# Kernel tuning notes

Hardware: AMD Instinct MI355X
Metric: run time of the kernel (lower is better)

## Reference

```python
import jax, jax.numpy as jnp
import numpy as np

ROUTING_ITERS = 3
EPS = 1e-12


def squash(s):
    # squash over both pose-matrix dims (axis=[-2,-1])
    n2 = jnp.sum(s * s, axis=(-2, -1), keepdims=True)
    n = jnp.sqrt(n2 + EPS)
    return s * (n2 / (1.0 + n2)) / n


def setup_inputs() -> dict:
    key = jax.random.key(0)
    k1, k2, k3 = jax.random.split(key, 3)
    B, I, O = 32, 4096, 32
    input_poses = jax.random.normal(k1, (B, I, 4, 4), dtype=jnp.float32)
    input_activations = jax.random.uniform(k2, (B, I), dtype=jnp.float32)
    # weight: [num_capsules, num_input_caps, 4, 4] (trans_in=trans_out=False for 4x4->4x4)
    w = jax.random.normal(k3, (O, I, 4, 4), dtype=jnp.float32) * 0.05
    return {"input_poses": input_poses, "input_activations": input_activations, "w": w}


def reference(input_poses, input_activations, w):
    # votes: expand_dims(poses,1) @ w, broadcast over output capsules -> [B,O,I,4,4]
    votes = jnp.einsum("bixy,oiyz->boixz", input_poses, w)
    B, O, I = votes.shape[0], votes.shape[1], votes.shape[2]

    # dynamic routing (routing-by-agreement)
    b = jnp.zeros((B, O, I), dtype=votes.dtype)
    s = None
    for it in range(ROUTING_ITERS):
        c = jax.nn.softmax(b, axis=1)  # couple over output capsules
        s = jnp.einsum("boi,boixy->boxy", c, votes)  # weighted sum [B,O,4,4]
        if it < ROUTING_ITERS - 1:
            v = squash(s)
            b = b + jnp.einsum("boixy,boxy->boi", votes, v)

    capsule_poses = squash(s)  # activation == 'squash'
    capsule_activations = jnp.sqrt(jnp.sum(capsule_poses * capsule_poses, axis=(-2, -1)) + EPS)
    return capsule_poses, capsule_activations
```

## Files before the change

### kernel.cpp

```cpp
#include <hip/hip_runtime.h>
#include <hip/hip_cooperative_groups.h>
#include <math.h>


#define NB 32
#define NI 4096
#define NO 32
#define I_TILE 16
#define NCHUNK (NI / I_TILE)
#define B_TILE 8
#define NBG (NB / B_TILE)
#define SOFF (NB * NO * 16)
#define EPSF 1e-12f

#define W_OSTR 10
#define W_ISTR (32 * W_OSTR)
#define W_WORDS (I_TILE * W_ISTR)
#define P_WORDS (B_TILE * I_TILE * 8)

namespace cg = cooperative_groups;

typedef _Float16 v2h __attribute__((ext_vector_type(2)));

#if __has_builtin(__builtin_amdgcn_fdot2)
__device__ __forceinline__ float fdot2(v2h a, v2h b, float c) {
    return __builtin_amdgcn_fdot2(a, b, c, false);
}
#else
__device__ __forceinline__ float fdot2(v2h a, v2h b, float c) {
    return fmaf((float)a.x, (float)b.x, fmaf((float)a.y, (float)b.y, c));
}
#endif

#if __has_builtin(__builtin_amdgcn_cvt_pkrtz)
__device__ __forceinline__ v2h pk2h(float a, float b) {
    return __builtin_bit_cast(v2h, __builtin_amdgcn_cvt_pkrtz(a, b));
}
#else
__device__ __forceinline__ v2h pk2h(float a, float b) {
    v2h r; r.x = (_Float16)a; r.y = (_Float16)b; return r;
}
#endif

__device__ __forceinline__ v2h bch(unsigned u) {
    return __builtin_bit_cast(v2h, u);
}

__device__ __forceinline__ float dot4(const float4 a, const float4 b) {
    return fmaf(a.x, b.x, fmaf(a.y, b.y, fmaf(a.z, b.z, a.w * b.w)));
}

__device__ __forceinline__ void fma4(float4& s, const float c, const float4 t) {
    s.x = fmaf(c, t.x, s.x);
    s.y = fmaf(c, t.y, s.y);
    s.z = fmaf(c, t.z, s.z);
    s.w = fmaf(c, t.w, s.w);
}

__device__ __forceinline__ void add4(float4& s, const float4 t) {
    s.x += t.x; s.y += t.y; s.z += t.z; s.w += t.w;
}

template <int CTRL>
__device__ __forceinline__ float dpp_add(float x) {
    int xi = __builtin_bit_cast(int, x);
    int yi = __builtin_amdgcn_update_dpp(0, xi, CTRL, 0xf, 0xf, false);
    return x + __builtin_bit_cast(float, yi);
}

__device__ __forceinline__ float sum32(float x) {
    x = dpp_add<0xB1>(x);
    x = dpp_add<0x4E>(x);
    x = dpp_add<0x141>(x);
    x = dpp_add<0x140>(x);
#if __has_builtin(__builtin_amdgcn_permlane16_swap)
    typedef unsigned uv2 __attribute__((ext_vector_type(2)));
    const unsigned xi = __builtin_bit_cast(unsigned, x);
    uv2 r = __builtin_amdgcn_permlane16_swap(xi, xi, false, false);
    return __builtin_bit_cast(float, r.x) + __builtin_bit_cast(float, r.y);
#else
    int t = __builtin_amdgcn_ds_swizzle(__builtin_bit_cast(int, x), 0x401F);
    return x + __builtin_bit_cast(float, t);
#endif
}

__global__ __launch_bounds__(256, 4) void caps_fused(
    const float* __restrict__ poses, const float* __restrict__ w,
    float* __restrict__ s_part, float* __restrict__ v_contrib,
    float* __restrict__ out)
{
    __shared__ unsigned wsw[W_WORDS];
    __shared__ unsigned psw[P_WORDS];
    __shared__ float red[16][17];

    const int tid    = threadIdx.x;
    const int chunk  = blockIdx.x;
    const int bgroup = blockIdx.y;
    const int ibase  = chunk * I_TILE;

    #pragma unroll
    for (int r = 0; r < 4; ++r) {
        const int idx = r * 256 + tid;
        const int o_l = idx >> 5;
        const int l   = idx & 31;
        const int i_l = l >> 1;
        const int m   = l & 1;
        const float* g = w + (((size_t)o_l * NI + ibase + i_l) << 4) + (m << 3);
        const float4 A = *(const float4*)g;
        const float4 B = *(const float4*)(g + 4);
        const v2h c0 = pk2h(A.x, B.x), c1 = pk2h(A.y, B.y);
        const v2h c2 = pk2h(A.z, B.z), c3 = pk2h(A.w, B.w);
        const int base = i_l * W_ISTR + o_l * W_OSTR + (m << 2);
        *(uint2*)&wsw[base]     = make_uint2(__builtin_bit_cast(unsigned, c0),
                                             __builtin_bit_cast(unsigned, c1));
        *(uint2*)&wsw[base + 2] = make_uint2(__builtin_bit_cast(unsigned, c2),
                                             __builtin_bit_cast(unsigned, c3));
    }
    #pragma unroll
    for (int r = 0; r < 2; ++r) {
        const int idx = r * 256 + tid;
        const int b_l = idx >> 6;
        const int l   = idx & 63;
        const int i_l = l >> 2;
        const int x   = l & 3;
        const float4 row = *(const float4*)(
            poses + (((size_t)(bgroup * B_TILE + b_l) * NI + ibase + i_l) << 4)
                  + (x << 2));
        const v2h c0 = pk2h(row.x, row.y), c1 = pk2h(row.z, row.w);
        *(uint2*)&psw[((b_l * I_TILE + i_l) << 3) + (x << 1)] =
            make_uint2(__builtin_bit_cast(unsigned, c0),
                       __builtin_bit_cast(unsigned, c1));
    }

    const int o    = tid & 31;
    const int bsub = tid >> 5;
    const int b    = bgroup * B_TILE + bsub;
    const int bo   = b * NO + o;
    const int rbo  = bgroup * NCHUNK + chunk;

    const unsigned* wrow = &wsw[o * W_OSTR];
    const unsigned* prow = &psw[(bsub * I_TILE) << 3];

    float4 vv0 = {0,0,0,0}, vv1 = {0,0,0,0}, vv2 = {0,0,0,0}, vv3 = {0,0,0,0};

    cg::grid_group gg = cg::this_grid();

    __syncthreads();

    for (int pass = 0; pass < 3; ++pass) {
        float4 s0 = {0,0,0,0}, s1 = {0,0,0,0}, s2 = {0,0,0,0}, s3 = {0,0,0,0};

        #pragma unroll 2
        for (int i = 0; i < I_TILE; ++i) {
            const uint2 wa = *(const uint2*)&wrow[i * W_ISTR + 0];
            const uint2 wb = *(const uint2*)&wrow[i * W_ISTR + 2];
            const uint2 wc = *(const uint2*)&wrow[i * W_ISTR + 4];
            const uint2 wd = *(const uint2*)&wrow[i * W_ISTR + 6];
            const uint4 pa = *(const uint4*)&prow[(i << 3) + 0];
            const uint4 pb = *(const uint4*)&prow[(i << 3) + 4];

            const v2h p00 = bch(pa.x), p01 = bch(pa.y);
            const v2h p10 = bch(pa.z), p11 = bch(pa.w);
            const v2h p20 = bch(pb.x), p21 = bch(pb.y);
            const v2h p30 = bch(pb.z), p31 = bch(pb.w);
            const v2h w00 = bch(wa.x), w01 = bch(wa.y);
            const v2h w02 = bch(wb.x), w03 = bch(wb.y);
            const v2h w10 = bch(wc.x), w11 = bch(wc.y);
            const v2h w12 = bch(wd.x), w13 = bch(wd.y);

            float4 t0, t1, t2, t3;
            t0.x = fdot2(p00, w00, fdot2(p01, w10, 0.0f));
            t0.y = fdot2(p00, w01, fdot2(p01, w11, 0.0f));
            t0.z = fdot2(p00, w02, fdot2(p01, w12, 0.0f));
            t0.w = fdot2(p00, w03, fdot2(p01, w13, 0.0f));
            t1.x = fdot2(p10, w00, fdot2(p11, w10, 0.0f));
            t1.y = fdot2(p10, w01, fdot2(p11, w11, 0.0f));
            t1.z = fdot2(p10, w02, fdot2(p11, w12, 0.0f));
            t1.w = fdot2(p10, w03, fdot2(p11, w13, 0.0f));
            t2.x = fdot2(p20, w00, fdot2(p21, w10, 0.0f));
            t2.y = fdot2(p20, w01, fdot2(p21, w11, 0.0f));
            t2.z = fdot2(p20, w02, fdot2(p21, w12, 0.0f));
            t2.w = fdot2(p20, w03, fdot2(p21, w13, 0.0f));
            t3.x = fdot2(p30, w00, fdot2(p31, w10, 0.0f));
            t3.y = fdot2(p30, w01, fdot2(p31, w11, 0.0f));
            t3.z = fdot2(p30, w02, fdot2(p31, w12, 0.0f));
            t3.w = fdot2(p30, w03, fdot2(p31, w13, 0.0f));

            float cc;
            if (pass == 0) {
                cc = 1.0f / 32.0f;
            } else {
                const float d = dot4(t0,vv0) + dot4(t1,vv1)
                              + dot4(t2,vv2) + dot4(t3,vv3);
                const float e  = __expf(d);
                const float es = sum32(e);
                cc = __fdividef(e, es);
            }
            fma4(s0, cc, t0); fma4(s1, cc, t1);
            fma4(s2, cc, t2); fma4(s3, cc, t3);
        }

        float4* sp = (float4*)(s_part + (((size_t)bo * NCHUNK + chunk) << 4));
        sp[0] = s0; sp[1] = s1; sp[2] = s2; sp[3] = s3;

        __threadfence();
        gg.sync();
        __threadfence();

        {
            const int k   = tid & 15;
            const int grp = tid >> 4;
            const float* base = s_part + ((size_t)rbo << 12);
            float acc = 0.0f;
            #pragma unroll
            for (int j = 0; j < 16; ++j)
                acc += base[((grp + (j << 4)) << 4) + k];
            red[grp][k] = acc;
        }
        __syncthreads();
        if (tid < 16) {
            float a = red[0][tid];
            #pragma unroll
            for (int g2 = 1; g2 < 16; ++g2) a += red[g2][tid];
            float x = a * a;
            #pragma unroll
            for (int msk = 8; msk >= 1; msk >>= 1)
                x += __shfl_xor(x, msk, 16);
            const float n2 = x;
            const float n  = sqrtf(n2 + EPSF);
            const float sc = (n2 / (1.0f + n2)) / n;
            if (pass < 2) {
                v_contrib[(rbo << 4) + tid] = sc * a;
            } else {
                out[(rbo << 4) + tid] = sc * a;
                if (tid == 0)
                    out[NB * NO * 16 + rbo] = sqrtf(n2 * sc * sc + EPSF);
            }
        }
        if (pass == 2) break;

        __threadfence();
        gg.sync();
        __threadfence();

        const float4* vp = (const float4*)(v_contrib + (bo << 4));
        add4(vv0, vp[0]); add4(vv1, vp[1]);
        add4(vv2, vp[2]); add4(vv3, vp[3]);
    }
}

__global__ __launch_bounds__(256, 4) void caps_pass_h(
    const float* __restrict__ poses, const float* __restrict__ w,
    const float* __restrict__ v_buf, float* __restrict__ s_part,
    const int pass)
{
    __shared__ unsigned wsw[W_WORDS];
    __shared__ unsigned psw[P_WORDS];
    const int tid    = threadIdx.x;
    const int chunk  = blockIdx.x;
    const int bgroup = blockIdx.y;
    const int ibase  = chunk * I_TILE;

    #pragma unroll
    for (int r = 0; r < 4; ++r) {
        const int idx = r * 256 + tid;
        const int o_l = idx >> 5;
        const int l   = idx & 31;
        const int i_l = l >> 1;
        const int m   = l & 1;
        const float* g = w + (((size_t)o_l * NI + ibase + i_l) << 4) + (m << 3);
        const float4 A = *(const float4*)g;
        const float4 B = *(const float4*)(g + 4);
        const v2h c0 = pk2h(A.x, B.x), c1 = pk2h(A.y, B.y);
        const v2h c2 = pk2h(A.z, B.z), c3 = pk2h(A.w, B.w);
        const int base = i_l * W_ISTR + o_l * W_OSTR + (m << 2);
        *(uint2*)&wsw[base]     = make_uint2(__builtin_bit_cast(unsigned, c0),
                                             __builtin_bit_cast(unsigned, c1));
        *(uint2*)&wsw[base + 2] = make_uint2(__builtin_bit_cast(unsigned, c2),
                                             __builtin_bit_cast(unsigned, c3));
    }
    #pragma unroll
    for (int r = 0; r < 2; ++r) {
        const int idx = r * 256 + tid;
        const int b_l = idx >> 6;
        const int l   = idx & 63;
        const int i_l = l >> 2;
        const int x   = l & 3;
        const float4 row = *(const float4*)(
            poses + (((size_t)(bgroup * B_TILE + b_l) * NI + ibase + i_l) << 4)
                  + (x << 2));
        const v2h c0 = pk2h(row.x, row.y), c1 = pk2h(row.z, row.w);
        *(uint2*)&psw[((b_l * I_TILE + i_l) << 3) + (x << 1)] =
            make_uint2(__builtin_bit_cast(unsigned, c0),
                       __builtin_bit_cast(unsigned, c1));
    }

    const int o    = tid & 31;
    const int bsub = tid >> 5;
    const int b    = bgroup * B_TILE + bsub;
    const int bo   = b * NO + o;

    float4 vv0 = {0,0,0,0}, vv1 = {0,0,0,0}, vv2 = {0,0,0,0}, vv3 = {0,0,0,0};
    if (pass > 0) {
        const float4* vp = (const float4*)(v_buf + (bo << 4));
        vv0 = vp[0]; vv1 = vp[1]; vv2 = vp[2]; vv3 = vp[3];
    }

    const unsigned* wrow = &wsw[o * W_OSTR];
    const unsigned* prow = &psw[(bsub * I_TILE) << 3];

    __syncthreads();

    float4 s0 = {0,0,0,0}, s1 = {0,0,0,0}, s2 = {0,0,0,0}, s3 = {0,0,0,0};

    #pragma unroll 2
    for (int i = 0; i < I_TILE; ++i) {
        const uint2 wa = *(const uint2*)&wrow[i * W_ISTR + 0];
        const uint2 wb = *(const uint2*)&wrow[i * W_ISTR + 2];
        const uint2 wc = *(const uint2*)&wrow[i * W_ISTR + 4];
        const uint2 wd = *(const uint2*)&wrow[i * W_ISTR + 6];
        const uint4 pa = *(const uint4*)&prow[(i << 3) + 0];
        const uint4 pb = *(const uint4*)&prow[(i << 3) + 4];

        const v2h p00 = bch(pa.x), p01 = bch(pa.y);
        const v2h p10 = bch(pa.z), p11 = bch(pa.w);
        const v2h p20 = bch(pb.x), p21 = bch(pb.y);
        const v2h p30 = bch(pb.z), p31 = bch(pb.w);
        const v2h w00 = bch(wa.x), w01 = bch(wa.y);
        const v2h w02 = bch(wb.x), w03 = bch(wb.y);
        const v2h w10 = bch(wc.x), w11 = bch(wc.y);
        const v2h w12 = bch(wd.x), w13 = bch(wd.y);

        float4 t0, t1, t2, t3;
        t0.x = fdot2(p00, w00, fdot2(p01, w10, 0.0f));
        t0.y = fdot2(p00, w01, fdot2(p01, w11, 0.0f));
        t0.z = fdot2(p00, w02, fdot2(p01, w12, 0.0f));
        t0.w = fdot2(p00, w03, fdot2(p01, w13, 0.0f));
        t1.x = fdot2(p10, w00, fdot2(p11, w10, 0.0f));
        t1.y = fdot2(p10, w01, fdot2(p11, w11, 0.0f));
        t1.z = fdot2(p10, w02, fdot2(p11, w12, 0.0f));
        t1.w = fdot2(p10, w03, fdot2(p11, w13, 0.0f));
        t2.x = fdot2(p20, w00, fdot2(p21, w10, 0.0f));
        t2.y = fdot2(p20, w01, fdot2(p21, w11, 0.0f));
        t2.z = fdot2(p20, w02, fdot2(p21, w12, 0.0f));
        t2.w = fdot2(p20, w03, fdot2(p21, w13, 0.0f));
        t3.x = fdot2(p30, w00, fdot2(p31, w10, 0.0f));
        t3.y = fdot2(p30, w01, fdot2(p31, w11, 0.0f));
        t3.z = fdot2(p30, w02, fdot2(p31, w12, 0.0f));
        t3.w = fdot2(p30, w03, fdot2(p31, w13, 0.0f));

        float cc;
        if (pass == 0) {
            cc = 1.0f / 32.0f;
        } else {
            const float d = dot4(t0,vv0) + dot4(t1,vv1)
                          + dot4(t2,vv2) + dot4(t3,vv3);
            const float e  = __expf(d);
            const float es = sum32(e);
            cc = __fdividef(e, es);
        }
        fma4(s0, cc, t0); fma4(s1, cc, t1);
        fma4(s2, cc, t2); fma4(s3, cc, t3);
    }

    float4* sp = (float4*)(s_part + ((size_t)chunk * (NB * NO) + bo) * 16);
    sp[0] = s0; sp[1] = s1; sp[2] = s2; sp[3] = s3;
}

__global__ __launch_bounds__(256) void caps_reduce(
    const float* __restrict__ s_part, float* __restrict__ v_buf,
    float* __restrict__ out, const int pass)
{
    const int e  = threadIdx.x & 63;
    const int c4 = threadIdx.x >> 6;
    const int eg = blockIdx.x * 64 + e;

    float acc = 0.0f;
    #pragma unroll 8
    for (int j = 0; j < NCHUNK / 4; ++j) {
        const int c = c4 * (NCHUNK / 4) + j;
        acc += s_part[(size_t)c * SOFF + eg];
    }
    __shared__ float red[4][64];
    red[c4][e] = acc;
    __syncthreads();

    if (threadIdx.x < 64) {
        const float a = red[0][e] + red[1][e] + red[2][e] + red[3][e];
        float x = a * a;
        #pragma unroll
        for (int msk = 8; msk >= 1; msk >>= 1)
            x += __shfl_xor(x, msk, 16);
        const float n2 = x;
        const float n  = sqrtf(n2 + EPSF);
        const float sc = (n2 / (1.0f + n2)) / n;
        if (pass < 2) {
            const float vold = (pass == 0) ? 0.0f : v_buf[eg];
            v_buf[eg] = fmaf(sc, a, vold);
        } else {
            out[eg] = sc * a;
            if ((e & 15) == 0)
                out[NB * NO * 16 + (eg >> 4)] = sqrtf(n2 * sc * sc + EPSF);
        }
    }
}

#define FB_CHUNKS 32
#define FB_IPB (NI / FB_CHUNKS)

__device__ __forceinline__ float4 row_mm(const float4 p, const float4 w0,
                                         const float4 w1, const float4 w2,
                                         const float4 w3) {
    float4 r;
    r.x = fmaf(p.x, w0.x, fmaf(p.y, w1.x, fmaf(p.z, w2.x, p.w * w3.x)));
    r.y = fmaf(p.x, w0.y, fmaf(p.y, w1.y, fmaf(p.z, w2.y, p.w * w3.y)));
    r.z = fmaf(p.x, w0.z, fmaf(p.y, w1.z, fmaf(p.z, w2.z, p.w * w3.z)));
    r.w = fmaf(p.x, w0.w, fmaf(p.y, w1.w, fmaf(p.z, w2.w, p.w * w3.w)));
    return r;
}

__global__ __launch_bounds__(256) void caps_pass_fb(
    const float* __restrict__ poses, const float* __restrict__ w,
    const float* __restrict__ v_buf, float* __restrict__ s_buf, const int mode)
{
    const int tid   = threadIdx.x;
    const int b     = blockIdx.y;
    const int chunk = blockIdx.x;
    const int o     = tid & 31;
    const int g     = tid >> 5;

    float4 v0 = {0,0,0,0}, v1 = {0,0,0,0}, v2 = {0,0,0,0}, v3 = {0,0,0,0};
    if (mode != 0) {
        const float4* vp = (const float4*)(v_buf + (((b * NO) + o) << 4));
        v0 = vp[0]; v1 = vp[1]; v2 = vp[2]; v3 = vp[3];
    }
    float4 s0 = {0,0,0,0}, s1 = {0,0,0,0}, s2 = {0,0,0,0}, s3 = {0,0,0,0};
    const int ibase = chunk * FB_IPB + g;
    #pragma unroll 4
    for (int it = 0; it < FB_IPB / 8; ++it) {
        const int i = ibase + (it << 3);
        const float4* ppf = (const float4*)(poses + ((((size_t)b * NI) + i) << 4));
        const float4 p0 = ppf[0], p1 = ppf[1], p2 = ppf[2], p3 = ppf[3];
        const float4* wpf = (const float4*)(w + ((((size_t)o * NI) + i) << 4));
        const float4 w0 = wpf[0], w1 = wpf[1], w2 = wpf[2], w3 = wpf[3];
        const float4 t0 = row_mm(p0, w0, w1, w2, w3);
        const float4 t1 = row_mm(p1, w0, w1, w2, w3);
        const float4 t2 = row_mm(p2, w0, w1, w2, w3);
        const float4 t3 = row_mm(p3, w0, w1, w2, w3);
        float cc;
        if (mode == 0) {
            cc = 1.0f / 32.0f;
        } else {
            float d = dot4(t0,v0) + dot4(t1,v1) + dot4(t2,v2) + dot4(t3,v3);
            const float e  = __expf(d);
            const float es = sum32(e);
            cc = __fdividef(e, es);
        }
        fma4(s0, cc, t0); fma4(s1, cc, t1);
        fma4(s2, cc, t2); fma4(s3, cc, t3);
    }
    __shared__ float red[8][32][16];
    float4* rp = (float4*)&red[g][o][0];
    rp[0] = s0; rp[1] = s1; rp[2] = s2; rp[3] = s3;
    __syncthreads();
    for (int idx = tid; idx < NO * 16; idx += 256) {
        const int oo = idx >> 4;
        const int k  = idx & 15;
        float acc = red[0][oo][k];
        #pragma unroll
        for (int gg = 1; gg < 8; ++gg) acc += red[gg][oo][k];
        atomicAdd(&s_buf[(((b * NO) + oo) << 4) + k], acc);
    }
}

__global__ __launch_bounds__(256) void caps_squash_fb(
    float* __restrict__ s_buf, float* __restrict__ v_buf,
    float* __restrict__ out, const int mode)
{
    const int idx = blockIdx.x * 256 + threadIdx.x;
    if (idx >= NB * NO) return;
    float4* sp = (float4*)(s_buf + (idx << 4));
    const float4 s0 = sp[0], s1 = sp[1], s2 = sp[2], s3 = sp[3];
    const float n2 = dot4(s0,s0) + dot4(s1,s1) + dot4(s2,s2) + dot4(s3,s3);
    const float n  = sqrtf(n2 + EPSF);
    const float sc = (n2 / (1.0f + n2)) / n;
    if (mode == 2) {
        float4* op = (float4*)(out + (idx << 4));
        op[0] = make_float4(sc*s0.x, sc*s0.y, sc*s0.z, sc*s0.w);
        op[1] = make_float4(sc*s1.x, sc*s1.y, sc*s1.z, sc*s1.w);
        op[2] = make_float4(sc*s2.x, sc*s2.y, sc*s2.z, sc*s2.w);
        op[3] = make_float4(sc*s3.x, sc*s3.y, sc*s3.z, sc*s3.w);
        out[NB * NO * 16 + idx] = sqrtf(n2 * sc * sc + EPSF);
    } else {
        float4* vp = (float4*)(v_buf + (idx << 4));
        float4 a0 = {0,0,0,0}, a1 = {0,0,0,0}, a2 = {0,0,0,0}, a3 = {0,0,0,0};
        if (mode != 0) { a0 = vp[0]; a1 = vp[1]; a2 = vp[2]; a3 = vp[3]; }
        vp[0] = make_float4(fmaf(sc,s0.x,a0.x), fmaf(sc,s0.y,a0.y), fmaf(sc,s0.z,a0.z), fmaf(sc,s0.w,a0.w));
        vp[1] = make_float4(fmaf(sc,s1.x,a1.x), fmaf(sc,s1.y,a1.y), fmaf(sc,s1.z,a1.z), fmaf(sc,s1.w,a1.w));
        vp[2] = make_float4(fmaf(sc,s2.x,a2.x), fmaf(sc,s2.y,a2.y), fmaf(sc,s2.z,a2.z), fmaf(sc,s2.w,a2.w));
        vp[3] = make_float4(fmaf(sc,s3.x,a3.x), fmaf(sc,s3.y,a3.y), fmaf(sc,s3.z,a3.z), fmaf(sc,s3.w,a3.w));
        const float4 z = {0,0,0,0};
        sp[0] = z; sp[1] = z; sp[2] = z; sp[3] = z;
    }
}

extern "C" void kernel_launch(void* const* d_in, const int* in_sizes, int n_in,
                              void* d_out, int out_size, void* d_ws, size_t ws_size,
                              hipStream_t stream) {
    (void)in_sizes; (void)n_in; (void)out_size;
    const float* poses = (const float*)d_in[0];
    const float* w     = (const float*)d_in[2];
    float* out = (float*)d_out;

    const size_t need = ((size_t)NCHUNK * SOFF + SOFF) * sizeof(float);
    if (ws_size >= need) {
        float* s_part = (float*)d_ws;
        float* v_buf  = s_part + (size_t)NCHUNK * SOFF;

        static int coop_state = -1;
        if (coop_state != 0) {
            void* args[] = { (void*)&poses, (void*)&w, (void*)&s_part,
                             (void*)&v_buf, (void*)&out };
            hipError_t e = hipLaunchCooperativeKernel(
                caps_fused, dim3(NCHUNK, NBG), dim3(256), args, 0u, stream);
            if (e == hipSuccess) { coop_state = 1; return; }
            coop_state = 0;
            (void)hipGetLastError();
        }

        dim3 gp(NCHUNK, NBG), blk(256), gr(256);
        for (int pass = 0; pass < 3; ++pass) {
            caps_pass_h<<<gp, blk, 0, stream>>>(poses, w, v_buf, s_part, pass);
            caps_reduce<<<gr, blk, 0, stream>>>(s_part, v_buf, out, pass);
        }
    } else {
        float* s_buf = (float*)d_ws;
        float* v_buf = s_buf + SOFF;
        (void)hipMemsetAsync(s_buf, 0, SOFF * sizeof(float), stream);
        dim3 grid(FB_CHUNKS, NB), block(256);
        for (int pass = 0; pass < 3; ++pass) {
            caps_pass_fb<<<grid, block, 0, stream>>>(poses, w, v_buf, s_buf, pass);
            caps_squash_fb<<<4, 256, 0, stream>>>(s_buf, v_buf, out, pass);
        }
    }
}
```

Measured before the change: 130.5 us.

## Replace cooperative grid sync with custom hierarchical atomic grid barrier

Drops the cooperative launch and cg grid sync in favour of a regular launch of a persistent kernel that synchronises through a two-level atomic counter barrier (32 leaf counters plus a root) with a generation flag. A small kernel zeroes the barrier state before each launch. The persistent path is taken only when the occupancy query reports enough resident blocks, since the regular launch gives no co-residency guarantee and could otherwise deadlock; a spin guard limits that risk. The fallback reduce kernel is also rewritten to use float4 loads and a 16-way split.

After: 128.3 us. About the same (-1.7%).

```diff
diff --git a/kernel.cpp b/kernel.cpp
--- a/kernel.cpp
+++ b/kernel.cpp
@@ -1,5 +1,4 @@
 #include <hip/hip_runtime.h>
-#include <hip/hip_cooperative_groups.h>
 #include <math.h>
 
 
@@ -10,6 +9,7 @@
 #define NCHUNK (NI / I_TILE)
 #define B_TILE 8
 #define NBG (NB / B_TILE)
+#define GRID_BLKS (NCHUNK * NBG)
 #define SOFF (NB * NO * 16)
 #define EPSF 1e-12f
 
@@ -18,7 +18,10 @@
 #define W_WORDS (I_TILE * W_ISTR)
 #define P_WORDS (B_TILE * I_TILE * 8)
 
-namespace cg = cooperative_groups;
+#define NLEAF 32
+#define LSTR 32
+#define BAR_EPOCH ((NLEAF + 1) * LSTR)
+#define BAR_WORDS (5 * BAR_EPOCH + LSTR)
 
 typedef _Float16 v2h __attribute__((ext_vector_type(2)));
 
@@ -84,10 +87,42 @@
 #endif
 }
 
-__global__ __launch_bounds__(256, 4) void caps_fused(
+__device__ __forceinline__ void grid_bar(unsigned* st, const int e,
+                                         const int bid) {
+    __syncthreads();
+    if (threadIdx.x == 0) {
+        __threadfence();
+        unsigned* base = st + (size_t)e * BAR_EPOCH;
+        unsigned* leaf = base + (size_t)(bid & (NLEAF - 1)) * LSTR;
+        unsigned* root = base + (size_t)NLEAF * LSTR;
+        unsigned* gen  = st + (size_t)5 * BAR_EPOCH;
+        if (atomicAdd(leaf, 1u) == (GRID_BLKS / NLEAF) - 1u) {
+            if (atomicAdd(root, 1u) == NLEAF - 1u) {
+                __threadfence();
+                __hip_atomic_store(gen, (unsigned)(e + 1), __ATOMIC_RELEASE,
+                                   __HIP_MEMORY_SCOPE_AGENT);
+            }
+        }
+        long guard = 0;
+        while (__hip_atomic_load(gen, __ATOMIC_ACQUIRE,
+                                 __HIP_MEMORY_SCOPE_AGENT) <= (unsigned)e) {
+            __builtin_amdgcn_s_sleep(2);
+            if (++guard > (1L << 27)) break;
+        }
+        __threadfence();
+    }
+    __syncthreads();
+}
+
+__global__ __launch_bounds__(256) void caps_bar_zero(unsigned* __restrict__ st) {
+    const int i = blockIdx.x * 256 + threadIdx.x;
+    if (i < BAR_WORDS) st[i] = 0u;
+}
+
+__global__ __launch_bounds__(256, 4) void caps_persist(
     const float* __restrict__ poses, const float* __restrict__ w,
     float* __restrict__ s_part, float* __restrict__ v_contrib,
-    float* __restrict__ out)
+    float* __restrict__ out, unsigned* __restrict__ bar)
 {
     __shared__ unsigned wsw[W_WORDS];
     __shared__ unsigned psw[P_WORDS];
@@ -96,6 +131,7 @@
     const int tid    = threadIdx.x;
     const int chunk  = blockIdx.x;
     const int bgroup = blockIdx.y;
+    const int bid    = bgroup * NCHUNK + chunk;
     const int ibase  = chunk * I_TILE;
 
     #pragma unroll
@@ -136,14 +172,12 @@
     const int bsub = tid >> 5;
     const int b    = bgroup * B_TILE + bsub;
     const int bo   = b * NO + o;
-    const int rbo  = bgroup * NCHUNK + chunk;
+    const int rbo  = bid;
 
     const unsigned* wrow = &wsw[o * W_OSTR];
     const unsigned* prow = &psw[(bsub * I_TILE) << 3];
 
     float4 vv0 = {0,0,0,0}, vv1 = {0,0,0,0}, vv2 = {0,0,0,0}, vv3 = {0,0,0,0};
-
-    cg::grid_group gg = cg::this_grid();
 
     __syncthreads();
 
@@ -203,9 +237,7 @@
         float4* sp = (float4*)(s_part + (((size_t)bo * NCHUNK + chunk) << 4));
         sp[0] = s0; sp[1] = s1; sp[2] = s2; sp[3] = s3;
 
-        __threadfence();
-        gg.sync();
-        __threadfence();
+        grid_bar(bar, 2 * pass, bid);
 
         {
             const int k   = tid & 15;
@@ -239,9 +271,7 @@
         }
         if (pass == 2) break;
 
-        __threadfence();
-        gg.sync();
-        __threadfence();
+        grid_bar(bar, 2 * pass + 1, bid);
 
         const float4* vp = (const float4*)(v_contrib + (bo << 4));
         add4(vv0, vp[0]); add4(vv1, vp[1]);
@@ -367,40 +397,47 @@
     sp[0] = s0; sp[1] = s1; sp[2] = s2; sp[3] = s3;
 }
 
-__global__ __launch_bounds__(256) void caps_reduce(
+__global__ __launch_bounds__(256) void caps_reduce4(
     const float* __restrict__ s_part, float* __restrict__ v_buf,
     float* __restrict__ out, const int pass)
 {
-    const int e  = threadIdx.x & 63;
-    const int c4 = threadIdx.x >> 6;
-    const int eg = blockIdx.x * 64 + e;
-
-    float acc = 0.0f;
-    #pragma unroll 8
-    for (int j = 0; j < NCHUNK / 4; ++j) {
-        const int c = c4 * (NCHUNK / 4) + j;
-        acc += s_part[(size_t)c * SOFF + eg];
-    }
-    __shared__ float red[4][64];
-    red[c4][e] = acc;
+    const int e   = threadIdx.x & 15;
+    const int grp = threadIdx.x >> 4;
+    const int v4g = blockIdx.x * 16 + e;
+
+    const float4* sp4 = (const float4*)s_part;
+    float4 acc = {0, 0, 0, 0};
+    #pragma unroll
+    for (int j = 0; j < NCHUNK / 16; ++j) {
+        const int c = grp + (j << 4);
+        add4(acc, sp4[(size_t)c * (SOFF / 4) + v4g]);
+    }
+
+    __shared__ float4 red4[16][17];
+    red4[grp][e] = acc;
     __syncthreads();
 
-    if (threadIdx.x < 64) {
-        const float a = red[0][e] + red[1][e] + red[2][e] + red[3][e];
-        float x = a * a;
+    if (threadIdx.x < 16) {
+        float4 a = red4[0][e];
         #pragma unroll
-        for (int msk = 8; msk >= 1; msk >>= 1)
-            x += __shfl_xor(x, msk, 16);
+        for (int g = 1; g < 16; ++g) add4(a, red4[g][e]);
+        float x = dot4(a, a);
+        x += __shfl_xor(x, 1, 4);
+        x += __shfl_xor(x, 2, 4);
         const float n2 = x;
         const float n  = sqrtf(n2 + EPSF);
         const float sc = (n2 / (1.0f + n2)) / n;
         if (pass < 2) {
-            const float vold = (pass == 0) ? 0.0f : v_buf[eg];
-            v_buf[eg] = fmaf(sc, a, vold);
+            float4* vp = (float4*)v_buf + v4g;
+            float4 vold = {0, 0, 0, 0};
+            if (pass > 0) vold = *vp;
+            *vp = make_float4(fmaf(sc, a.x, vold.x), fmaf(sc, a.y, vold.y),
+                              fmaf(sc, a.z, vold.z), fmaf(sc, a.w, vold.w));
         } else {
-            out[eg] = sc * a;
-            if ((e & 15) == 0)
-                out[NB * NO * 16 + (eg >> 4)] = sqrtf(n2 * sc * sc + EPSF);
+            ((float4*)out)[v4g] =
+                make_float4(sc * a.x, sc * a.y, sc * a.z, sc * a.w);
+            if ((e & 3) == 0)
+                out[NB * NO * 16 + (v4g >> 2)] = sqrtf(n2 * sc * sc + EPSF);
         }
     }
 }
@@ -512,26 +549,32 @@
     const float* w     = (const float*)d_in[2];
     float* out = (float*)d_out;
 
-    const size_t need = ((size_t)NCHUNK * SOFF + SOFF) * sizeof(float);
+    const size_t n_spart = (size_t)NCHUNK * SOFF;
+    const size_t need = (n_spart + SOFF) * 4 + BAR_WORDS * 4 + 256;
     if (ws_size >= need) {
-        float* s_part = (float*)d_ws;
-        float* v_buf  = s_part + (size_t)NCHUNK * SOFF;
-
-        static int coop_state = -1;
-        if (coop_state != 0) {
-            void* args[] = { (void*)&poses, (void*)&w, (void*)&s_part,
-                             (void*)&v_buf, (void*)&out };
-            hipError_t e = hipLaunchCooperativeKernel(
-                caps_fused, dim3(NCHUNK, NBG), dim3(256), args, 0u, stream);
-            if (e == hipSuccess) { coop_state = 1; return; }
-            coop_state = 0;
+        float*    s_part = (float*)d_ws;
+        float*    v_buf  = s_part + n_spart;
+        unsigned* bar    = (unsigned*)(v_buf + SOFF);
+
+        static int occ = -1;
+        if (occ < 0) {
+            int t = 0;
+            hipError_t e = hipOccupancyMaxActiveBlocksPerMultiprocessor(
+                &t, caps_persist, 256, 0);
+            occ = (e == hipSuccess) ? t : 0;
             (void)hipGetLastError();
         }
-
-        dim3 gp(NCHUNK, NBG), blk(256), gr(256);
-        for (int pass = 0; pass < 3; ++pass) {
-            caps_pass_h<<<gp, blk, 0, stream>>>(poses, w, v_buf, s_part, pass);
-            caps_reduce<<<gr, blk, 0, stream>>>(s_part, v_buf, out, pass);
+        if (occ >= 4) {
+            dim3 gp(NCHUNK, NBG), blk(256);
+            caps_bar_zero<<<(BAR_WORDS + 255) / 256, blk, 0, stream>>>(bar);
+            caps_persist<<<gp, blk, 0, stream>>>(poses, w, s_part, v_buf,
+                                                 out, bar);
+        } else {
+            dim3 gp(NCHUNK, NBG), blk(256), gr(256);
+            for (int pass = 0; pass < 3; ++pass) {
+                caps_pass_h<<<gp, blk, 0, stream>>>(poses, w, v_buf, s_part, pass);
+                caps_reduce4<<<gr, blk, 0, stream>>>(s_part, v_buf, out, pass);
+            }
         }
     } else {
         float* s_buf = (float*)d_ws;
```
